# Kernel tuning notes

Hardware: AMD Instinct MI355X
Metric: run time of the kernel (lower is better)

The kernel has to match this reference:

```python
import jax, jax.numpy as jnp
import numpy as np
from jax import lax

NEG = jnp.float32(-1e30)  # log-domain 'zero'
BLANK = 0


def setup_inputs() -> dict:
    T, N, C, S = 512, 512, 80, 128
    k0, k1, k2, k3 = jax.random.split(jax.random.key(0), 4)
    logits = jax.random.normal(k0, (T, N, C), dtype=jnp.float32)
    log_probs = jax.nn.log_softmax(logits, axis=-1)  # CTCLoss expects log-probs
    targets = jax.random.randint(k1, (N, S), 1, C).astype(jnp.int32)  # labels in [1, C-1], blank=0 excluded
    input_lengths = jax.random.randint(k2, (N,), T // 2, T + 1).astype(jnp.int32)
    target_lengths = jax.random.randint(k3, (N,), S // 2, S + 1).astype(jnp.int32)
    return {"log_probs": log_probs, "targets": targets,
            "input_lengths": input_lengths, "target_lengths": target_lengths}


def _ctc_loss(log_probs, targets, input_lengths, target_lengths):
    # log_probs: (T, N, C) log-probabilities; targets: (N, S) labels (no blanks)
    T, N, C = log_probs.shape
    S = targets.shape[1]
    L = 2 * S + 1  # extended label length: blank-interleaved

    # extended targets: [blank, y1, blank, y2, ..., yS, blank]  -> (N, L)
    ext = jnp.zeros((N, L), jnp.int32).at[:, 1::2].set(targets)
    # skip transition (s-2 -> s) allowed only if ext[s] != ext[s-2]
    # (blank positions have ext[s]==ext[s-2]==blank, so this also forbids blank skips)
    skip_ok = jnp.pad(ext[:, 2:] != ext[:, :-2], ((0, 0), (2, 0)), constant_values=False)

    # emission log-probs on the lattice: (T, N, L)
    emit = jnp.take_along_axis(log_probs, jnp.broadcast_to(ext[None], (T, N, L)), axis=2)

    # alpha at t=0: only lattice positions 0 (blank) and 1 (first label) reachable
    alpha0 = jnp.full((N, L), NEG).at[:, 0].set(emit[0, :, 0]).at[:, 1].set(emit[0, :, 1])

    def step(alpha, xs):
        em, t = xs  # em: (N, L)
        a1 = jnp.pad(alpha[:, :-1], ((0, 0), (1, 0)), constant_values=NEG)
        a2 = jnp.where(skip_ok,
                       jnp.pad(alpha[:, :-2], ((0, 0), (2, 0)), constant_values=NEG), NEG)
        m = jnp.maximum(alpha, jnp.maximum(a1, a2))
        lse = m + jnp.log(jnp.exp(alpha - m) + jnp.exp(a1 - m) + jnp.exp(a2 - m))
        new = lse + em
        # freeze alpha for finished sequences (t >= input_length)
        alpha_new = jnp.where((t < input_lengths)[:, None], new, alpha)
        return alpha_new, None

    alpha_T, _ = lax.scan(step, alpha0, (emit[1:], jnp.arange(1, T, dtype=jnp.int32)))

    # final states: last blank (2*tl) and last label (2*tl - 1)
    i1 = (2 * target_lengths)[:, None]
    v1 = jnp.take_along_axis(alpha_T, i1, axis=1)[:, 0]
    v2 = jnp.take_along_axis(alpha_T, i1 - 1, axis=1)[:, 0]
    m = jnp.maximum(v1, v2)
    loss = -(m + jnp.log(jnp.exp(v1 - m) + jnp.exp(v2 - m)))
    # zero_infinity=True: infeasible alignments -> 0 loss
    loss = jnp.where(jnp.isfinite(loss) & (loss < 1e10), loss, 0.0)
    return loss  # (N,) reduction='none'


def reference(log_probs, targets, input_lengths, target_lengths):
    return _ctc_loss(log_probs, targets, input_lengths, target_lengths)
```

## Files before the change

kernel.cpp:

```cpp
#include <hip/hip_runtime.h>


#define NEGC  (-1.0e30f)
#define LOG2E 1.4426950408889634f
#define LN2   0.6931471805599453f

constexpr int T_ = 512;
constexpr int C_ = 80;
constexpr int S_ = 128;
constexpr int U_ = 8;
constexpr int WROW = 520;

__device__ __forceinline__ float exp2a(float x) { return __builtin_amdgcn_exp2f(x); }
__device__ __forceinline__ float log2a(float x) { return __builtin_amdgcn_logf(x); }

template <int CTRL>
__device__ __forceinline__ float dppf(float old_, float src) {
    return __int_as_float(__builtin_amdgcn_update_dpp(
        __float_as_int(old_), __float_as_int(src), CTRL, 0xF, 0xF, false));
}

__device__ __forceinline__ int wave_max_bits(float m) {
    m = fmaxf(m, dppf<0x111>(m, m));
    m = fmaxf(m, dppf<0x112>(m, m));
    m = fmaxf(m, dppf<0x114>(m, m));
    m = fmaxf(m, dppf<0x118>(m, m));
    m = fmaxf(m, dppf<0x142>(m, m));
    m = fmaxf(m, dppf<0x143>(m, m));
    return __builtin_amdgcn_readlane(__float_as_int(m), 63);
}

__device__ __forceinline__ float lse2(float x, float y) {
    float m = fmaxf(x, y);
    return m + log2a(1.0f + exp2a(-fabsf(x - y)));
}
__device__ __forceinline__ float lse3(float x, float y, float z) {
    float m = fmaxf(x, fmaxf(y, z));
    return m + log2a(exp2a(x - m) + exp2a(y - m) + exp2a(z - m));
}

__global__ __launch_bounds__(64, 1) void ctc_half(
    const float* __restrict__ lp, const int* __restrict__ tgt,
    const int* __restrict__ ilen, const int* __restrict__ tlen,
    float* __restrict__ ws, int N)
{
    const int b   = blockIdx.x;
    const int n   = b >> 1;
    const int dir = b & 1;
    const int l   = threadIdx.x;

    __shared__ float lds[1280];

    float* ga = ws + (size_t)n * WROW;
    float* gg = ga + 260;

    const int* tn = tgt + n * S_;
    const int ext1 = tn[2 * l];
    const int ext3 = tn[2 * l + 1];
    const int prev = (l > 0) ? tn[2 * l - 1] : 0;
    const bool skip1 = (l > 0) && (ext1 != prev);
    const bool skip3 = (ext3 != ext1);
    const bool skb3  = (l < 63) && (tn[2 * l + 2] != ext3);

    int len = ilen[n];
    len = len < 1 ? 1 : (len > T_ ? T_ : len);
    const int mid = len >> 1;

    const int irst = N * C_;
    const float* lpn = lp + (size_t)n * C_;

    int dkr[10], ckk[10];
    #pragma unroll
    for (int k = 0; k < 10; ++k) {
        const unsigned flat = (unsigned)l + 64u * k;
        const unsigned dk = flat / 80u;
        ckk[k] = (int)(flat - 80u * dk);
        dkr[k] = (int)dk * irst;
    }

    float VA[10], VB[10];
    float ebA[8], e1A[8], e3A[8];
    float ebB[8], e1B[8], e3B[8];

#define SISSUE_F(FB, V) do {                                                   \
    const int s_ = (FB) * irst;                                                \
    _Pragma("unroll")                                                          \
    for (int k = 0; k < 10; ++k)                                               \
        V[k] = lpn[(unsigned)(s_ + dkr[k] + ckk[k])];                          \
} while (0)

#define SISSUE_B(FB, V) do {                                                   \
    const int s_ = (FB) * irst;                                                \
    _Pragma("unroll")                                                          \
    for (int k = 0; k < 10; ++k) {                                             \
        int v_ = s_ - dkr[k]; v_ = v_ < 0 ? 0 : v_;                            \
        V[k] = lpn[(unsigned)(v_ + ckk[k])];                                   \
    }                                                                          \
} while (0)

#define SWRITE(H, V) do {                                                      \
    _Pragma("unroll")                                                          \
    for (int k = 0; k < 10; ++k)                                               \
        lds[(H) * 640 + l + 64 * k] = V[k] * LOG2E;                            \
} while (0)

#define RLOAD(H, EB, E1, E3) do {                                              \
    _Pragma("unroll")                                                          \
    for (int u = 0; u < 8; ++u) {                                              \
        const int base_ = (H) * 640 + u * 80;                                  \
        EB[u] = lds[base_];                                                    \
        E1[u] = lds[base_ + ext1];                                             \
        E3[u] = lds[base_ + ext3];                                             \
    }                                                                          \
} while (0)

#define RENORM(S0, S1, S2, S3, S4) do {                                        \
    const int mi_ = wave_max_bits(                                             \
        fmaxf(fmaxf(fmaxf(S0, S1), fmaxf(S2, S3)), S4));                       \
    const int e_ = (mi_ > 0) ? (((mi_ >> 23) & 255) - 187) : 0;                \
    E += e_;                                                                   \
    S0 = ldexpf(S0, -e_); S1 = ldexpf(S1, -e_); S2 = ldexpf(S2, -e_);          \
    S3 = ldexpf(S3, -e_); S4 = ldexpf(S4, -e_);                                \
} while (0)

#define COMP8_F(TB, EB, E1, E3) do {                                           \
    float Pb_ = exp2a(EB[0]), Q1_ = exp2a(E1[0]), Q3_ = exp2a(E3[0]);          \
    _Pragma("unroll")                                                          \
    for (int u = 0; u < 8; ++u) {                                              \
        const int t_ = (TB) + u;                                               \
        float PbN_ = 0.f, Q1N_ = 0.f, Q3N_ = 0.f;                              \
        if (u < 7) {                                                           \
            PbN_ = exp2a(EB[u + 1]); Q1N_ = exp2a(E1[u + 1]);                  \
            Q3N_ = exp2a(E3[u + 1]);                                           \
        }                                                                      \
        if (t_ < mid) {                                                        \
            const float sm1_ = dppf<0x138>(0.0f, p3_);      \
            const float i0_ = p0_ + sm1_;                                      \
            const float i1_ = p1_ + p0_ + (skip1 ? sm1_ : 0.f);                \
            const float i2_ = p2_ + p1_;                                       \
            const float i3_ = p3_ + p2_ + (skip3 ? p1_ : 0.f);                 \
            const float i4_ = p4_ + p3_;                                       \
            p0_ = i0_ * Pb_; p1_ = i1_ * Q1_; p2_ = i2_ * Pb_;                 \
            p3_ = i3_ * Q3_; p4_ = i4_ * Pb_;                                  \
        }                                                                      \
        if (u < 7) { Pb_ = PbN_; Q1_ = Q1N_; Q3_ = Q3N_; }                     \
    }                                                                          \
} while (0)

#define COMP8_B(TB, EB, E1, E3) do {                                           \
    float Pb_ = exp2a(EB[0]), Q1_ = exp2a(E1[0]), Q3_ = exp2a(E3[0]);          \
    _Pragma("unroll")                                                          \
    for (int u = 0; u < 8; ++u) {                                              \
        const int t_ = (TB) - u;                                               \
        float PbN_ = 0.f, Q1N_ = 0.f, Q3N_ = 0.f;                              \
        if (u < 7) {                                                           \
            PbN_ = exp2a(EB[u + 1]); Q1N_ = exp2a(E1[u + 1]);                  \
            Q3N_ = exp2a(E3[u + 1]);                                           \
        }                                                                      \
        if (t_ >= mid) {                                                       \
            const float x0_ = dppf<0x130>(g4_, g0_);    \
            const float x1_ = dppf<0x130>(0.f, g1_);    \
            const float i0_ = g0_ + g1_;                                       \
            const float i1_ = g1_ + g2_ + (skip3 ? g3_ : 0.f);                 \
            const float i2_ = g2_ + g3_;                                       \
            const float i3_ = g3_ + x0_ + (skb3 ? x1_ : 0.f);                  \
            g0_ = i0_ * Pb_; g1_ = i1_ * Q1_; g2_ = i2_ * Pb_;                 \
            g3_ = i3_ * Q3_; g4_ = g4_ * Pb_;                                  \
        }                                                                      \
        if (u < 7) { Pb_ = PbN_; Q1_ = Q1N_; Q3_ = Q3N_; }                     \
    }                                                                          \
} while (0)

    if (dir == 0) {
        SISSUE_F(1, VA);  SWRITE(0, VA);
        SISSUE_F(9, VB);  SWRITE(1, VB);
        SISSUE_F(17, VA);
        RLOAD(0, ebA, e1A, e3A);

        float p0_ = 0.f, p1_ = 0.f, p2_ = 0.f, p3_ = 0.f, p4_ = 0.f;
        int   E = -60;
        if (l == 0) {
            p0_ = exp2a(lpn[0] * LOG2E + 60.0f);
            p1_ = exp2a(lpn[ext1] * LOG2E + 60.0f);
        }
        for (int tb = 1; tb < mid; tb += 16) {
            RLOAD(1, ebB, e1B, e3B);
            COMP8_F(tb, ebA, e1A, e3A);
            RENORM(p0_, p1_, p2_, p3_, p4_);
            SWRITE(0, VA);
            SISSUE_F(tb + 24, VB);
            RLOAD(0, ebA, e1A, e3A);
            COMP8_F(tb + 8, ebB, e1B, e3B);
            RENORM(p0_, p1_, p2_, p3_, p4_);
            SWRITE(1, VB);
            SISSUE_F(tb + 32, VA);
        }
        const float fE = (float)E;
        ga[4 * l + 0] = (p0_ > 0.f) ? fmaxf(log2a(p0_) + fE, NEGC) : NEGC;
        ga[4 * l + 1] = (p1_ > 0.f) ? fmaxf(log2a(p1_) + fE, NEGC) : NEGC;
        ga[4 * l + 2] = (p2_ > 0.f) ? fmaxf(log2a(p2_) + fE, NEGC) : NEGC;
        ga[4 * l + 3] = (p3_ > 0.f) ? fmaxf(log2a(p3_) + fE, NEGC) : NEGC;
        if (l == 63) ga[256] = (p4_ > 0.f) ? fmaxf(log2a(p4_) + fE, NEGC) : NEGC;
    } else {
        const int fe = len - 1;
        SISSUE_B(fe - 1, VA);  SWRITE(0, VA);
        SISSUE_B(fe - 9, VB);  SWRITE(1, VB);
        SISSUE_B(fe - 17, VA);
        RLOAD(0, ebA, e1A, e3A);

        const int tl = tlen[n];
        const int sA = 2 * tl, sB = 2 * tl - 1;
        float g0_, g1_, g2_, g3_, g4_;
        int E = -60;
        {
            const unsigned feo = (unsigned)(fe * irst);
            const float ebi = lpn[feo] * LOG2E + 60.0f;
            const float e1i = lpn[feo + ext1] * LOG2E + 60.0f;
            const float e3i = lpn[feo + ext3] * LOG2E + 60.0f;
            const int s0 = 4 * l;
            g0_ = (s0     == sA)                 ? exp2a(ebi) : 0.f;
            g1_ = (s0 + 1 == sA || s0 + 1 == sB) ? exp2a(e1i) : 0.f;
            g2_ = (s0 + 2 == sA)                 ? exp2a(ebi) : 0.f;
            g3_ = (s0 + 3 == sA || s0 + 3 == sB) ? exp2a(e3i) : 0.f;
            g4_ = (l == 63 && 256 == sA)         ? exp2a(ebi) : 0.f;
        }
        for (int tb = fe - 1; tb >= mid; tb -= 16) {
            RLOAD(1, ebB, e1B, e3B);
            COMP8_B(tb, ebA, e1A, e3A);
            RENORM(g0_, g1_, g2_, g3_, g4_);
            SWRITE(0, VA);
            SISSUE_B(tb - 24, VB);
            RLOAD(0, ebA, e1A, e3A);
            COMP8_B(tb - 8, ebB, e1B, e3B);
            RENORM(g0_, g1_, g2_, g3_, g4_);
            SWRITE(1, VB);
            SISSUE_B(tb - 32, VA);
        }
        const float fE = (float)E;
        gg[4 * l + 0] = (g0_ > 0.f) ? fmaxf(log2a(g0_) + fE, NEGC) : NEGC;
        gg[4 * l + 1] = (g1_ > 0.f) ? fmaxf(log2a(g1_) + fE, NEGC) : NEGC;
        gg[4 * l + 2] = (g2_ > 0.f) ? fmaxf(log2a(g2_) + fE, NEGC) : NEGC;
        gg[4 * l + 3] = (g3_ > 0.f) ? fmaxf(log2a(g3_) + fE, NEGC) : NEGC;
        if (l == 63) gg[256] = (g4_ > 0.f) ? fmaxf(log2a(g4_) + fE, NEGC) : NEGC;
    }
#undef COMP8_F
#undef COMP8_B
#undef SISSUE_F
#undef SISSUE_B
#undef SWRITE
#undef RLOAD
#undef RENORM
}

__global__ __launch_bounds__(64) void ctc_comb(
    const float* __restrict__ ws, const int* __restrict__ tgt,
    const int* __restrict__ ilen, const int* __restrict__ tlen,
    float* __restrict__ out, int N)
{
    const int n = blockIdx.x;
    const int l = threadIdx.x;
    const float* ga = ws + (size_t)n * WROW;
    const float* gg = ga + 260;

    int len = ilen[n];
    len = len < 1 ? 1 : (len > T_ ? T_ : len);
    const int tl = tlen[n];

    if (len == 1) {
        if (l == 0) {
            const float v1 = ga[2 * tl];
            const float v2 = (2 * tl >= 1) ? ga[2 * tl - 1] : NEGC;
            float loss = -lse2(v1, v2) * LN2;
            if (!(loss < 1e10f) || !isfinite(loss)) loss = 0.0f;
            out[n] = loss;
        }
        return;
    }

    const int* tn = tgt + n * S_;
    const int ext1 = tn[2 * l];
    const int ext3 = tn[2 * l + 1];
    const int prev = (l > 0) ? tn[2 * l - 1] : 0;
    const bool skip1 = (l > 0) && (ext1 != prev);
    const bool skip3 = (ext3 != ext1);

    const int s0 = 4 * l;
    const float Am1 = (l > 0) ? ga[s0 - 1] : NEGC;
    const float A0 = ga[s0], A1 = ga[s0 + 1], A2 = ga[s0 + 2], A3 = ga[s0 + 3];
    const float v0 = lse2(A0, Am1)                    + gg[s0];
    const float v1 = lse3(A1, A0, skip1 ? Am1 : NEGC) + gg[s0 + 1];
    const float v2 = lse2(A2, A1)                     + gg[s0 + 2];
    const float v3 = lse3(A3, A2, skip3 ? A1 : NEGC)  + gg[s0 + 3];
    const float v4 = (l == 63) ? (lse2(ga[256], A3) + gg[256]) : NEGC;

    float m = fmaxf(fmaxf(v0, v1), fmaxf(fmaxf(v2, v3), v4));
    float ssum = exp2a(v0 - m) + exp2a(v1 - m) + exp2a(v2 - m)
               + exp2a(v3 - m) + exp2a(v4 - m);
    float M = m;
    #pragma unroll
    for (int d = 1; d < 64; d <<= 1) M = fmaxf(M, __shfl_xor(M, d));
    float r = ssum * exp2a(m - M);
    #pragma unroll
    for (int d = 1; d < 64; d <<= 1) r += __shfl_xor(r, d);
    if (l == 0) {
        float loss = -LN2 * (M + log2a(r));
        if (!(loss < 1e10f) || !isfinite(loss)) loss = 0.0f;
        out[n] = loss;
    }
}

__global__ __launch_bounds__(128) void ctc_fused(
    const float* __restrict__ lp, const int* __restrict__ tgt,
    const int* __restrict__ ilen, const int* __restrict__ tlen,
    float* __restrict__ out, int N)
{
    const int n    = blockIdx.x;
    const int wave = threadIdx.x >> 6;
    const int l    = threadIdx.x & 63;

    __shared__ float ga[2 * S_ + 1];
    __shared__ float gg[2 * S_ + 1];

    const int* tn = tgt + n * S_;
    const int ext1 = tn[2 * l];
    const int ext3 = tn[2 * l + 1];
    const int prev = (l > 0) ? tn[2 * l - 1] : 0;
    const bool skip1 = (l > 0) && (ext1 != prev);
    const bool skip3 = (ext3 != ext1);
    const bool skb1 = (tn[2 * l + 1] != tn[2 * l]);
    const bool skb3 = (l < 63) && (tn[2 * l + 2] != tn[2 * l + 1]);

    int len = ilen[n];
    len = len < 1 ? 1 : (len > T_ ? T_ : len);
    const int mid = len >> 1;

    const size_t rstride = (size_t)N * C_;
    const float* lpn = lp + (size_t)n * C_;
    const float* pB = lpn;
    const float* p1 = lpn + ext1;
    const float* p3 = lpn + ext3;

    float rb[U_], r1[U_], r3[U_];

    if (wave == 0) {
        const int last = mid - 1 > 0 ? mid - 1 : 0;
        #pragma unroll
        for (int u = 0; u < U_; ++u) {
            const int r = u + 1;
            const int rc = r < mid ? r : last;
            const size_t o = (size_t)rc * rstride;
            rb[r & 7] = pB[o]; r1[r & 7] = p1[o]; r3[r & 7] = p3[o];
        }
        float a0 = NEGC, a1 = NEGC, a2 = NEGC, a3 = NEGC, a4 = NEGC;
        {
            const float i0 = pB[0] * LOG2E;
            const float i1 = p1[0] * LOG2E;
            if (l == 0) { a0 = i0; a1 = i1; }
        }
        for (int tb = 1; tb < mid; tb += U_) {
            #pragma unroll
            for (int u = 0; u < U_; ++u) {
                const int t = tb + u;
                const int slot = (1 + u) & 7;
                const float eb = rb[slot] * LOG2E;
                const float e1 = r1[slot] * LOG2E;
                const float e3 = r3[slot] * LOG2E;
                const int rr = t + U_;
                const int rc = rr < mid ? rr : last;
                const size_t o = (size_t)rc * rstride;
                const float nrb = pB[o], nr1 = p1[o], nr3 = p3[o];
                if (t < mid) {
                    const float sm1 = dppf<0x138>(NEGC, a3);
                    const float z1 = skip1 ? sm1 : NEGC;
                    const float z3 = skip3 ? a1  : NEGC;
                    const float n0 = lse2(a0, sm1)    + eb;
                    const float n1 = lse3(a1, a0, z1) + e1;
                    const float n2 = lse2(a2, a1)     + eb;
                    const float n3 = lse3(a3, a2, z3) + e3;
                    const float n4 = lse2(a4, a3)     + eb;
                    a0 = n0; a1 = n1; a2 = n2; a3 = n3; a4 = n4;
                }
                rb[slot] = nrb; r1[slot] = nr1; r3[slot] = nr3;
            }
        }
        ga[4 * l + 0] = a0; ga[4 * l + 1] = a1;
        ga[4 * l + 2] = a2; ga[4 * l + 3] = a3;
        if (l == 63) ga[256] = a4;
    } else {
        const int fe = len - 1;
        #pragma unroll
        for (int u = 0; u < U_; ++u) {
            int rc = fe - 1 - u; if (rc < 0) rc = 0;
            const size_t o = (size_t)rc * rstride;
            rb[u] = pB[o]; r1[u] = p1[o]; r3[u] = p3[o];
        }
        const int tl = tlen[n];
        const int sA = 2 * tl, sB = 2 * tl - 1;
        float g0, g1, g2, g3, g4;
        {
            const size_t o = (size_t)fe * rstride;
            const float ebi = pB[o] * LOG2E;
            const float e1i = p1[o] * LOG2E;
            const float e3i = p3[o] * LOG2E;
            const int s0 = 4 * l;
            g0 = (s0     == sA)                 ? ebi : NEGC;
            g1 = (s0 + 1 == sA || s0 + 1 == sB) ? e1i : NEGC;
            g2 = (s0 + 2 == sA)                 ? ebi : NEGC;
            g3 = (s0 + 3 == sA || s0 + 3 == sB) ? e3i : NEGC;
            g4 = (l == 63 && 256 == sA)         ? ebi : NEGC;
        }
        for (int tb = fe - 1; tb >= mid; tb -= U_) {
            #pragma unroll
            for (int u = 0; u < U_; ++u) {
                const int t = tb - u;
                const int slot = ((fe - 1 - tb) + u) & 7;
                const float eb = rb[slot] * LOG2E;
                const float e1 = r1[slot] * LOG2E;
                const float e3 = r3[slot] * LOG2E;
                int rc = t - U_; if (rc < 0) rc = 0;
                const size_t o = (size_t)rc * rstride;
                const float nrb = pB[o], nr1 = p1[o], nr3 = p3[o];
                if (t >= mid) {
                    const float nx0 = dppf<0x130>(g4,   g0);
                    const float nx1 = dppf<0x130>(NEGC, g1);
                    const float z1 = skb1 ? g3  : NEGC;
                    const float z3 = skb3 ? nx1 : NEGC;
                    const float n0 = lse2(g0, g1)      + eb;
                    const float n1 = lse3(g1, g2, z1)  + e1;
                    const float n2 = lse2(g2, g3)      + eb;
                    const float n3 = lse3(g3, nx0, z3) + e3;
                    const float n4 = g4 + eb;
                    g0 = n0; g1 = n1; g2 = n2; g3 = n3; g4 = n4;
                }
                rb[slot] = nrb; r1[slot] = nr1; r3[slot] = nr3;
            }
        }
        gg[4 * l + 0] = g0; gg[4 * l + 1] = g1;
        gg[4 * l + 2] = g2; gg[4 * l + 3] = g3;
        if (l == 63) gg[256] = g4;
    }

    __syncthreads();

    if (wave == 0) {
        const int tl = tlen[n];
        if (len == 1) {
            if (l == 0) {
                const float v1 = ga[2 * tl];
                const float v2 = (2 * tl >= 1) ? ga[2 * tl - 1] : NEGC;
                float loss = -lse2(v1, v2) * LN2;
                if (!(loss < 1e10f) || !isfinite(loss)) loss = 0.0f;
                out[n] = loss;
            }
            return;
        }
        const int s0 = 4 * l;
        const float Am1 = (l > 0) ? ga[s0 - 1] : NEGC;
        const float A0 = ga[s0], A1 = ga[s0 + 1], A2 = ga[s0 + 2], A3 = ga[s0 + 3];
        const float v0 = lse2(A0, Am1)                    + gg[s0];
        const float v1 = lse3(A1, A0, skip1 ? Am1 : NEGC) + gg[s0 + 1];
        const float v2 = lse2(A2, A1)                     + gg[s0 + 2];
        const float v3 = lse3(A3, A2, skip3 ? A1 : NEGC)  + gg[s0 + 3];
        const float v4 = (l == 63) ? (lse2(ga[256], A3) + gg[256]) : NEGC;

        float m = fmaxf(fmaxf(v0, v1), fmaxf(fmaxf(v2, v3), v4));
        float ssum = exp2a(v0 - m) + exp2a(v1 - m) + exp2a(v2 - m)
                   + exp2a(v3 - m) + exp2a(v4 - m);
        float M = m;
        #pragma unroll
        for (int d = 1; d < 64; d <<= 1) M = fmaxf(M, __shfl_xor(M, d));
        float r = ssum * exp2a(m - M);
        #pragma unroll
        for (int d = 1; d < 64; d <<= 1) r += __shfl_xor(r, d);
        if (l == 0) {
            float loss = -LN2 * (M + log2a(r));
            if (!(loss < 1e10f) || !isfinite(loss)) loss = 0.0f;
            out[n] = loss;
        }
    }
}

extern "C" void kernel_launch(void* const* d_in, const int* in_sizes, int n_in,
                              void* d_out, int out_size, void* d_ws, size_t ws_size,
                              hipStream_t stream) {
    const float* lp  = (const float*)d_in[0];
    const int*   tg  = (const int*)  d_in[1];
    const int*   il  = (const int*)  d_in[2];
    const int*   tl  = (const int*)  d_in[3];
    float*       out = (float*)d_out;
    const int N = in_sizes[2];
    const size_t need = (size_t)N * WROW * sizeof(float);
    if (ws_size >= need) {
        ctc_half<<<2 * N, 64, 0, stream>>>(lp, tg, il, tl, (float*)d_ws, N);
        ctc_comb<<<N, 64, 0, stream>>>((const float*)d_ws, tg, il, tl, out, N);
    } else {
        ctc_fused<<<N, 128, 0, stream>>>(lp, tg, il, tl, out, N);
    }
}
```

Measured before the change: 132.3 us.

## Precompute exp2 at LDS staging and interleave LDS reads into recurrence

Emission exponentiation moves from the serial recurrence into the LDS write stage, so each lane does 10 exp2 per 8 steps instead of 24, and these sit off the dependency chain. LDS reads for the next 8-step block are interleaved into the current block's compute loop. Global prefetch is deepened from one block ahead to two. Skip selects become fma with 0/1 multipliers. The cost is higher register pressure from the extra prefetch buffers, and overflow behaviour changes slightly because exponentials are taken before renormalization.

```diff
diff --git a/kernel.cpp b/kernel.cpp
--- a/kernel.cpp
+++ b/kernel.cpp
@@ -61,6 +61,9 @@
     const bool skip1 = (l > 0) && (ext1 != prev);
     const bool skip3 = (ext3 != ext1);
     const bool skb3  = (l < 63) && (tn[2 * l + 2] != ext3);
+    const float k1f  = skip1 ? 1.0f : 0.0f;
+    const float k3f  = skip3 ? 1.0f : 0.0f;
+    const float kb3f = skb3  ? 1.0f : 0.0f;
 
     int len = ilen[n];
     len = len < 1 ? 1 : (len > T_ ? T_ : len);
@@ -101,7 +104,7 @@
 #define SWRITE(H, V) do {                                                      \
     _Pragma("unroll")                                                          \
     for (int k = 0; k < 10; ++k)                                               \
-        lds[(H) * 640 + l + 64 * k] = V[k] * LOG2E;                            \
+        lds[(H) * 640 + l + 64 * k] = exp2a(V[k] * LOG2E);                     \
 } while (0)
 
 #define RLOAD(H, EB, E1, E3) do {                                              \
@@ -123,58 +126,50 @@
     S3 = ldexpf(S3, -e_); S4 = ldexpf(S4, -e_);                                \
 } while (0)
 
-#define COMP8_F(TB, EB, E1, E3) do {                                           \
-    float Pb_ = exp2a(EB[0]), Q1_ = exp2a(E1[0]), Q3_ = exp2a(E3[0]);          \
+#define COMP8_F(TB, CEB, CE1, CE3, RH, NEB, NE1, NE3) do {                     \
     _Pragma("unroll")                                                          \
     for (int u = 0; u < 8; ++u) {                                              \
         const int t_ = (TB) + u;                                               \
-        float PbN_ = 0.f, Q1N_ = 0.f, Q3N_ = 0.f;                              \
-        if (u < 7) {                                                           \
-            PbN_ = exp2a(EB[u + 1]); Q1N_ = exp2a(E1[u + 1]);                  \
-            Q3N_ = exp2a(E3[u + 1]);                                           \
-        }                                                                      \
+        const int rb_ = (RH) * 640 + u * 80;                                   \
+        NEB[u] = lds[rb_]; NE1[u] = lds[rb_ + ext1]; NE3[u] = lds[rb_ + ext3]; \
         if (t_ < mid) {                                                        \
+            const float Pb_ = CEB[u], Q1_ = CE1[u], Q3_ = CE3[u];              \
             const float sm1_ = dppf<0x138>(0.0f, p3_);      \
             const float i0_ = p0_ + sm1_;                                      \
-            const float i1_ = p1_ + p0_ + (skip1 ? sm1_ : 0.f);                \
+            const float i1_ = fmaf(sm1_, k1f, p1_ + p0_);                      \
             const float i2_ = p2_ + p1_;                                       \
-            const float i3_ = p3_ + p2_ + (skip3 ? p1_ : 0.f);                 \
+            const float i3_ = fmaf(p1_, k3f, p3_ + p2_);                       \
             const float i4_ = p4_ + p3_;                                       \
             p0_ = i0_ * Pb_; p1_ = i1_ * Q1_; p2_ = i2_ * Pb_;                 \
             p3_ = i3_ * Q3_; p4_ = i4_ * Pb_;                                  \
         }                                                                      \
-        if (u < 7) { Pb_ = PbN_; Q1_ = Q1N_; Q3_ = Q3N_; }                     \
     }                                                                          \
 } while (0)
 
-#define COMP8_B(TB, EB, E1, E3) do {                                           \
-    float Pb_ = exp2a(EB[0]), Q1_ = exp2a(E1[0]), Q3_ = exp2a(E3[0]);          \
+#define COMP8_B(TB, CEB, CE1, CE3, RH, NEB, NE1, NE3) do {                     \
     _Pragma("unroll")                                                          \
     for (int u = 0; u < 8; ++u) {                                              \
         const int t_ = (TB) - u;                                               \
-        float PbN_ = 0.f, Q1N_ = 0.f, Q3N_ = 0.f;                              \
-        if (u < 7) {                                                           \
-            PbN_ = exp2a(EB[u + 1]); Q1N_ = exp2a(E1[u + 1]);                  \
-            Q3N_ = exp2a(E3[u + 1]);                                           \
-        }                                                                      \
+        const int rb_ = (RH) * 640 + u * 80;                                   \
+        NEB[u] = lds[rb_]; NE1[u] = lds[rb_ + ext1]; NE3[u] = lds[rb_ + ext3]; \
         if (t_ >= mid) {                                                       \
+            const float Pb_ = CEB[u], Q1_ = CE1[u], Q3_ = CE3[u];              \
             const float x0_ = dppf<0x130>(g4_, g0_);    \
             const float x1_ = dppf<0x130>(0.f, g1_);    \
             const float i0_ = g0_ + g1_;                                       \
-            const float i1_ = g1_ + g2_ + (skip3 ? g3_ : 0.f);                 \
+            const float i1_ = fmaf(g3_, k3f, g1_ + g2_);                       \
             const float i2_ = g2_ + g3_;                                       \
-            const float i3_ = g3_ + x0_ + (skb3 ? x1_ : 0.f);                  \
+            const float i3_ = fmaf(x1_, kb3f, g3_ + x0_);                      \
             g0_ = i0_ * Pb_; g1_ = i1_ * Q1_; g2_ = i2_ * Pb_;                 \
             g3_ = i3_ * Q3_; g4_ = g4_ * Pb_;                                  \
         }                                                                      \
-        if (u < 7) { Pb_ = PbN_; Q1_ = Q1N_; Q3_ = Q3N_; }                     \
     }                                                                          \
 } while (0)
 
     if (dir == 0) {
-        SISSUE_F(1, VA);  SWRITE(0, VA);
-        SISSUE_F(9, VB);  SWRITE(1, VB);
-        SISSUE_F(17, VA);
+        SISSUE_F(1, VA);  SISSUE_F(9, VB);
+        SWRITE(0, VA);    SWRITE(1, VB);
+        SISSUE_F(17, VA); SISSUE_F(25, VB);
         RLOAD(0, ebA, e1A, e3A);
 
         float p0_ = 0.f, p1_ = 0.f, p2_ = 0.f, p3_ = 0.f, p4_ = 0.f;
@@ -184,16 +179,14 @@
             p1_ = exp2a(lpn[ext1] * LOG2E + 60.0f);
         }
         for (int tb = 1; tb < mid; tb += 16) {
-            RLOAD(1, ebB, e1B, e3B);
-            COMP8_F(tb, ebA, e1A, e3A);
+            COMP8_F(tb, ebA, e1A, e3A, 1, ebB, e1B, e3B);
             RENORM(p0_, p1_, p2_, p3_, p4_);
             SWRITE(0, VA);
-            SISSUE_F(tb + 24, VB);
-            RLOAD(0, ebA, e1A, e3A);
-            COMP8_F(tb + 8, ebB, e1B, e3B);
+            SISSUE_F(tb + 32, VA);
+            COMP8_F(tb + 8, ebB, e1B, e3B, 0, ebA, e1A, e3A);
             RENORM(p0_, p1_, p2_, p3_, p4_);
             SWRITE(1, VB);
-            SISSUE_F(tb + 32, VA);
+            SISSUE_F(tb + 40, VB);
         }
         const float fE = (float)E;
         ga[4 * l + 0] = (p0_ > 0.f) ? fmaxf(log2a(p0_) + fE, NEGC) : NEGC;
@@ -203,9 +196,9 @@
         if (l == 63) ga[256] = (p4_ > 0.f) ? fmaxf(log2a(p4_) + fE, NEGC) : NEGC;
     } else {
         const int fe = len - 1;
-        SISSUE_B(fe - 1, VA);  SWRITE(0, VA);
-        SISSUE_B(fe - 9, VB);  SWRITE(1, VB);
-        SISSUE_B(fe - 17, VA);
+        SISSUE_B(fe - 1, VA);  SISSUE_B(fe - 9, VB);
+        SWRITE(0, VA);         SWRITE(1, VB);
+        SISSUE_B(fe - 17, VA); SISSUE_B(fe - 25, VB);
         RLOAD(0, ebA, e1A, e3A);
 
         const int tl = tlen[n];
@@ -225,16 +218,14 @@
             g4_ = (l == 63 && 256 == sA)         ? exp2a(ebi) : 0.f;
         }
         for (int tb = fe - 1; tb >= mid; tb -= 16) {
-            RLOAD(1, ebB, e1B, e3B);
-            COMP8_B(tb, ebA, e1A, e3A);
+            COMP8_B(tb, ebA, e1A, e3A, 1, ebB, e1B, e3B);
             RENORM(g0_, g1_, g2_, g3_, g4_);
             SWRITE(0, VA);
-            SISSUE_B(tb - 24, VB);
-            RLOAD(0, ebA, e1A, e3A);
-            COMP8_B(tb - 8, ebB, e1B, e3B);
+            SISSUE_B(tb - 32, VA);
+            COMP8_B(tb - 8, ebB, e1B, e3B, 0, ebA, e1A, e3A);
             RENORM(g0_, g1_, g2_, g3_, g4_);
             SWRITE(1, VB);
-            SISSUE_B(tb - 32, VA);
+            SISSUE_B(tb - 40, VB);
         }
         const float fE = (float)E;
         gg[4 * l + 0] = (g0_ > 0.f) ? fmaxf(log2a(g0_) + fE, NEGC) : NEGC;
```

After: 133.1 us. No clear change (+0.6%).
